# Optimization experiments

Measured on AMD Instinct MI355X. Metric: run time of the kernel, lower is better.

## Reference

```python
import jax, jax.numpy as jnp
import numpy as np

NUM_BINS = 30
MIN_BW = 1e-3
MIN_BH = 1e-3
MIN_D = 1e-3
LO_IN, HI_IN = 0.0, 1.0
LO_OUT, HI_OUT = 0.0, 1.0
DERIV_OUT_LO = (HI_OUT - LO_OUT) / (HI_IN - LO_IN)  # default outside derivatives
DERIV_OUT_HI = DERIV_OUT_LO
EPS = 1e-6
B, V = 65536, 64


def _cumparams(unnorm, lo, hi, min_size):
    # softmax bin sizes with a floor, cumsum into knot positions. [V,K] -> ([V,K+1],[V,K])
    K = unnorm.shape[-1]
    p = jax.nn.softmax(unnorm, axis=-1)
    p = min_size + (1.0 - min_size * K) * p
    cp = jnp.cumsum(p, axis=-1)
    cp = jnp.pad(cp, [(0, 0), (1, 0)])
    cp = (hi - lo) * cp + lo
    cp = cp.at[..., 0].set(lo).at[..., -1].set(hi)
    sizes = cp[..., 1:] - cp[..., :-1]
    return cp, sizes


def setup_inputs() -> dict:
    key = jax.random.key(0)
    k0, k1, k2, k3 = jax.random.split(key, 4)
    return {
        "inputs": jax.random.uniform(k0, (B, V), dtype=jnp.float32),
        "unnormalized_widths": jax.random.uniform(k1, (V, NUM_BINS), dtype=jnp.float32),
        "unnormalized_heights": jax.random.uniform(k2, (V, NUM_BINS), dtype=jnp.float32),
        "unnormalized_derivatives": jax.random.uniform(k3, (V, NUM_BINS - 1), dtype=jnp.float32),
    }


def reference(inputs, unnormalized_widths, unnormalized_heights, unnormalized_derivatives):
    K = NUM_BINS
    nb, nv = inputs.shape

    cumw, widths = _cumparams(unnormalized_widths, LO_IN, HI_IN, MIN_BW)      # [V,K+1],[V,K]
    cumh, heights = _cumparams(unnormalized_heights, LO_OUT, HI_OUT, MIN_BH)  # [V,K+1],[V,K]

    # boundary derivatives pinned so softplus(const)+MIN_D == 1
    const = float(np.log(np.exp(1.0 - MIN_D) - 1.0))
    ud = jnp.pad(unnormalized_derivatives, [(0, 0), (1, 1)], constant_values=const)
    derivs = MIN_D + jax.nn.softplus(ud)  # [V,K+1]
    delta = heights / widths              # [V,K]

    # per-element bin search (forward mode -> search in cumwidths)
    bounds = cumw.at[..., -1].add(EPS)                                   # [V,K+1]
    bin_idx = jnp.sum(inputs[..., None] >= bounds[None], axis=-1) - 1    # [B,V]
    bin_idx = jnp.clip(bin_idx, 0, K - 1)

    vidx = jnp.arange(nv)[None, :]  # broadcast variable index [1,V]
    icw = cumw[vidx, bin_idx]       # input_cumwidths [B,V]
    ibw = widths[vidx, bin_idx]
    ich = cumh[vidx, bin_idx]
    idl = delta[vidx, bin_idx]
    d0 = derivs[vidx, bin_idx]
    d1 = derivs[vidx, bin_idx + 1]
    ih = heights[vidx, bin_idx]

    theta = (inputs - icw) / ibw
    t1mt = theta * (1.0 - theta)
    numerator = ih * (idl * theta * theta + d0 * t1mt)
    denominator = idl + (d0 + d1 - 2.0 * idl) * t1mt
    spline_out = ich + numerator / denominator
    deriv_num = idl * idl * (d1 * theta * theta + 2.0 * idl * t1mt + d0 * (1.0 - theta) ** 2)
    spline_lad = jnp.log(deriv_num) - 2.0 * jnp.log(denominator)

    below = inputs < LO_IN
    above = inputs > HI_IN
    inside = ~(below | above)
    out_lo = LO_OUT + (inputs - LO_IN) * DERIV_OUT_LO
    out_hi = HI_OUT + (inputs - HI_IN) * DERIV_OUT_HI
    outputs = jnp.where(below, out_lo, jnp.where(above, out_hi, spline_out))
    logabsdet = jnp.where(inside, spline_lad, 0.0)
    return outputs, logabsdet
```

## Files before the change

kernel.cpp:

```cpp
#include <hip/hip_runtime.h>
#include <math.h>


#define NB 65536
#define NV 64
#define NKB 30
#define REC_D 124
#define DER_BASE 7936
#define DER_S 33
#define LUT_BASE_B 40192
#define LUT_S 132
#define TOT_D 12160
#define GRID 768
#define BSZ 512

__global__ __launch_bounds__(64) void rqs_params(const float* __restrict__ uw,
                                                 const float* __restrict__ uh,
                                                 const float* __restrict__ ud,
                                                 float* __restrict__ P) {
  const int v = blockIdx.x;
  const int lane = threadIdx.x;
  const float MINB = 1e-3f;
  const float scale = 1.0f - MINB * (float)NKB;

  float cw_e, winv, wnxt;
  {
    float u = (lane < NKB) ? uw[v * NKB + lane] : -1e30f;
    float m = u;
#pragma unroll
    for (int s = 32; s >= 1; s >>= 1) m = fmaxf(m, __shfl_xor(m, s));
    float e = (lane < NKB) ? expf(u - m) : 0.0f;
    float t = e;
#pragma unroll
    for (int s = 32; s >= 1; s >>= 1) t += __shfl_xor(t, s);
    float pk = (lane < NKB) ? (MINB + scale * (e / t)) : 0.0f;
    float ci = pk;
#pragma unroll
    for (int s = 1; s < 64; s <<= 1) {
      float z = __shfl_up(ci, s);
      if (lane >= s) ci += z;
    }
    cw_e = ci - pk;
    wnxt = (lane == NKB - 1) ? 1.0f : ci;
    winv = 1.0f / (wnxt - cw_e);
  }
  float ch_e, hh;
  {
    float u = (lane < NKB) ? uh[v * NKB + lane] : -1e30f;
    float m = u;
#pragma unroll
    for (int s = 32; s >= 1; s >>= 1) m = fmaxf(m, __shfl_xor(m, s));
    float e = (lane < NKB) ? expf(u - m) : 0.0f;
    float t = e;
#pragma unroll
    for (int s = 32; s >= 1; s >>= 1) t += __shfl_xor(t, s);
    float pk = (lane < NKB) ? (MINB + scale * (e / t)) : 0.0f;
    float ci = pk;
#pragma unroll
    for (int s = 1; s < 64; s <<= 1) {
      float z = __shfl_up(ci, s);
      if (lane >= s) ci += z;
    }
    ch_e = ci - pk;
    float hnxt = (lane == NKB - 1) ? 1.0f : ci;
    hh = hnxt - ch_e;
  }
  if (lane < NKB) {
    float4 r = {cw_e, winv, ch_e, hh};
    *(float4*)(P + v * REC_D + 4 * lane) = r;
  }
  if (lane == NKB) {
    float4 r = {1.0f + 1e-6f, 0.0f, 0.0f, 0.0f};
    *(float4*)(P + v * REC_D + 4 * NKB) = r;
  }
  {
    const float CST = (float)log(exp(1.0 - 1e-3) - 1.0);
    if (lane <= NKB) {
      float x = (lane == 0 || lane == NKB) ? CST : ud[v * (NKB - 1) + lane - 1];
      float sp = (x > 0.f) ? (x + log1pf(expf(-x))) : log1pf(expf(x));
      P[DER_BASE + v * DER_S + lane] = 1e-3f + sp;
    }
  }
  {
    float t0 = (float)lane * (1.0f / 128.0f);
    float t1 = (float)(lane + 64) * (1.0f / 128.0f);
    int lo0 = 0, lo1 = 0;
#pragma unroll
    for (int kk = 0; kk < NKB; ++kk) {
      float c = __shfl(wnxt, kk);
      lo0 += (c <= t0) ? 1 : 0;
      lo1 += (c <= t1) ? 1 : 0;
    }
    unsigned char* lb = (unsigned char*)P + LUT_BASE_B + v * LUT_S;
    lb[lane] = (unsigned char)lo0;
    lb[lane + 64] = (unsigned char)lo1;
  }
}

__global__ __launch_bounds__(BSZ, 6) void rqs_main(const float* __restrict__ x,
                                                   const float* __restrict__ P,
                                                   float* __restrict__ out) {
  __shared__ __align__(16) float lds[TOT_D];
  for (int i = threadIdx.x; i < TOT_D / 4; i += BSZ)
    ((float4*)lds)[i] = ((const float4*)P)[i];
  __syncthreads();
  const unsigned char* lutb = (const unsigned char*)lds;

  const int N = NB * NV;
  const int n4 = N / 4;
  for (int gid = blockIdx.x * BSZ + threadIdx.x; gid < n4; gid += GRID * BSZ) {
    float4 xv = ((const float4*)x)[gid];
    const int v0 = (gid & 15) * 4;
    float xs[4] = {xv.x, xv.y, xv.z, xv.w};
    float o[4], l[4];
#pragma unroll
    for (int j = 0; j < 4; ++j) {
      float xx = xs[j];
      const int vj = v0 + j;
      int u = (int)(xx * 128.0f);
      u = u < 0 ? 0 : (u > 127 ? 127 : u);
      int lo = lutb[LUT_BASE_B + vj * LUT_S + u];
      float probe = lds[vj * REC_D + 4 * (lo + 1)];
      int b = lo + ((xx >= probe) ? 1 : 0);
      b = b > 29 ? 29 : b;
      float4 r4 = *(const float4*)&lds[vj * REC_D + 4 * b];
      float d0 = lds[DER_BASE + vj * DER_S + b];
      float d1 = lds[DER_BASE + vj * DER_S + b + 1];
      float icw = r4.x, winv = r4.y, ich = r4.z, ih = r4.w;
      float idl  = ih * winv;
      float th   = (xx - icw) * winv;
      float omt  = 1.0f - th;
      float t1mt = th * omt;
      float th2  = th * th;
      float num  = ih * (idl * th2 + d0 * t1mt);
      float den  = idl + (d0 + d1 - 2.0f * idl) * t1mt;
      float rden = __builtin_amdgcn_rcpf(den);
      float so   = ich + num * rden;
      float dn   = idl * idl * (d1 * th2 + 2.0f * idl * t1mt + d0 * omt * omt);
      float sl   = __logf(dn * rden * rden);
      bool inside = !(xx < 0.0f) && !(xx > 1.0f);
      o[j] = inside ? so : xx;
      l[j] = inside ? sl : 0.0f;
    }
    float4 ov = {o[0], o[1], o[2], o[3]};
    float4 lv = {l[0], l[1], l[2], l[3]};
    ((float4*)out)[gid] = ov;
    ((float4*)(out + N))[gid] = lv;
  }
}

extern "C" void kernel_launch(void* const* d_in, const int* in_sizes, int n_in,
                              void* d_out, int out_size, void* d_ws, size_t ws_size,
                              hipStream_t stream) {
  const float* x  = (const float*)d_in[0];
  const float* uw = (const float*)d_in[1];
  const float* uh = (const float*)d_in[2];
  const float* ud = (const float*)d_in[3];
  float* out = (float*)d_out;
  float* P   = (float*)d_ws;

  rqs_params<<<NV, 64, 0, stream>>>(uw, uh, ud, P);
  rqs_main<<<GRID, BSZ, 0, stream>>>(x, P, out);
}
```

Baseline: 85.40 us.

## Fuse parameter kernel into main kernel and embed knot fraction in LUT

Merges the per-variable parameter kernel into the main kernel, so every block recomputes the softmax, cumsum, softplus and LUT for all 64 variables directly into LDS. This removes a second launch and the global workspace round-trip. Each LUT entry now packs a 16-bit fractional knot position alongside the bin index, so the probe comparison no longer needs a second LDS read. Grid drops to 512 blocks with occupancy hint 4, and per-variable base offsets are hoisted out of the loop. In exchange, each block repeats the parameter work and the LDS footprint grows, and the quantized probe could in rare cases pick a different bin than the exact knot.

```diff
diff --git a/kernel.cpp b/kernel.cpp
--- a/kernel.cpp
+++ b/kernel.cpp
@@ -8,130 +8,146 @@
 #define REC_D 124
 #define DER_BASE 7936
 #define DER_S 33
-#define LUT_BASE_B 40192
-#define LUT_S 132
-#define TOT_D 12160
-#define GRID 768
+#define LUTD_BASE 10048
+#define LUT_S 133
+#define TOT_D 18560
+#define GRID 512
 #define BSZ 512
 
-__global__ __launch_bounds__(64) void rqs_params(const float* __restrict__ uw,
-                                                 const float* __restrict__ uh,
-                                                 const float* __restrict__ ud,
-                                                 float* __restrict__ P) {
-  const int v = blockIdx.x;
-  const int lane = threadIdx.x;
+__global__ __launch_bounds__(BSZ, 4) void rqs_fused(const float* __restrict__ x,
+                                                    const float* __restrict__ uw,
+                                                    const float* __restrict__ uh,
+                                                    const float* __restrict__ ud,
+                                                    float* __restrict__ out) {
+  __shared__ __align__(16) float lds[TOT_D];
+  const int tid = threadIdx.x;
+  const int wave = tid >> 6;
+  const int lane = tid & 63;
+  const int half = lane >> 5;
+  const int hl = lane & 31;
   const float MINB = 1e-3f;
   const float scale = 1.0f - MINB * (float)NKB;
 
-  float cw_e, winv, wnxt;
-  {
-    float u = (lane < NKB) ? uw[v * NKB + lane] : -1e30f;
+  for (int p = 0; p < 4; ++p) {
+    const int v = wave * 8 + p * 2 + half;
+    float u = (hl < NKB) ? uw[v * NKB + hl] : -1e30f;
     float m = u;
 #pragma unroll
-    for (int s = 32; s >= 1; s >>= 1) m = fmaxf(m, __shfl_xor(m, s));
-    float e = (lane < NKB) ? expf(u - m) : 0.0f;
+    for (int s = 16; s >= 1; s >>= 1) m = fmaxf(m, __shfl_xor(m, s));
+    float e = (hl < NKB) ? expf(u - m) : 0.0f;
     float t = e;
 #pragma unroll
-    for (int s = 32; s >= 1; s >>= 1) t += __shfl_xor(t, s);
-    float pk = (lane < NKB) ? (MINB + scale * (e / t)) : 0.0f;
+    for (int s = 16; s >= 1; s >>= 1) t += __shfl_xor(t, s);
+    float pk = (hl < NKB) ? (MINB + scale * (e / t)) : 0.0f;
     float ci = pk;
 #pragma unroll
-    for (int s = 1; s < 64; s <<= 1) {
+    for (int s = 1; s < 32; s <<= 1) {
       float z = __shfl_up(ci, s);
-      if (lane >= s) ci += z;
+      if (hl >= s) ci += z;
     }
-    cw_e = ci - pk;
-    wnxt = (lane == NKB - 1) ? 1.0f : ci;
-    winv = 1.0f / (wnxt - cw_e);
-  }
-  float ch_e, hh;
-  {
-    float u = (lane < NKB) ? uh[v * NKB + lane] : -1e30f;
-    float m = u;
+    float cw_e = ci - pk;
+    float wnxt = (hl == NKB - 1) ? 1.0f : ci;
+    float winv = 1.0f / (wnxt - cw_e);
+    float uhv = (hl < NKB) ? uh[v * NKB + hl] : -1e30f;
+    float mh = uhv;
 #pragma unroll
-    for (int s = 32; s >= 1; s >>= 1) m = fmaxf(m, __shfl_xor(m, s));
-    float e = (lane < NKB) ? expf(u - m) : 0.0f;
-    float t = e;
+    for (int s = 16; s >= 1; s >>= 1) mh = fmaxf(mh, __shfl_xor(mh, s));
+    float eh = (hl < NKB) ? expf(uhv - mh) : 0.0f;
+    float th = eh;
 #pragma unroll
-    for (int s = 32; s >= 1; s >>= 1) t += __shfl_xor(t, s);
-    float pk = (lane < NKB) ? (MINB + scale * (e / t)) : 0.0f;
-    float ci = pk;
+    for (int s = 16; s >= 1; s >>= 1) th += __shfl_xor(th, s);
+    float pkh = (hl < NKB) ? (MINB + scale * (eh / th)) : 0.0f;
+    float cih = pkh;
 #pragma unroll
-    for (int s = 1; s < 64; s <<= 1) {
-      float z = __shfl_up(ci, s);
-      if (lane >= s) ci += z;
+    for (int s = 1; s < 32; s <<= 1) {
+      float z = __shfl_up(cih, s);
+      if (hl >= s) cih += z;
     }
-    ch_e = ci - pk;
-    float hnxt = (lane == NKB - 1) ? 1.0f : ci;
-    hh = hnxt - ch_e;
-  }
-  if (lane < NKB) {
-    float4 r = {cw_e, winv, ch_e, hh};
-    *(float4*)(P + v * REC_D + 4 * lane) = r;
-  }
-  if (lane == NKB) {
-    float4 r = {1.0f + 1e-6f, 0.0f, 0.0f, 0.0f};
-    *(float4*)(P + v * REC_D + 4 * NKB) = r;
-  }
-  {
-    const float CST = (float)log(exp(1.0 - 1e-3) - 1.0);
-    if (lane <= NKB) {
-      float x = (lane == 0 || lane == NKB) ? CST : ud[v * (NKB - 1) + lane - 1];
-      float sp = (x > 0.f) ? (x + log1pf(expf(-x))) : log1pf(expf(x));
-      P[DER_BASE + v * DER_S + lane] = 1e-3f + sp;
+    float ch_e = cih - pkh;
+    float hnxt = (hl == NKB - 1) ? 1.0f : cih;
+    float hh = hnxt - ch_e;
+    if (hl < NKB) {
+      float4 r = {cw_e, winv, ch_e, hh};
+      *(float4*)(lds + v * REC_D + 4 * hl) = r;
+    }
+    {
+      const float CST = (float)log(exp(1.0 - 1e-3) - 1.0);
+      if (hl <= NKB) {
+        float xd = (hl == 0 || hl == NKB) ? CST : ud[v * (NKB - 1) + hl - 1];
+        float sp = (xd > 0.f) ? (xd + log1pf(expf(-xd))) : log1pf(expf(xd));
+        lds[DER_BASE + v * DER_S + hl] = 1e-3f + sp;
+      }
+    }
+    {
+      float tb[4];
+      int lo[4];
+#pragma unroll
+      for (int q = 0; q < 4; ++q) {
+        tb[q] = (float)(hl + 32 * q) * (1.0f / 128.0f);
+        lo[q] = 0;
+      }
+      for (int kk = 0; kk < NKB - 1; ++kk) {
+        float c = __shfl(wnxt, (half << 5) + kk);
+#pragma unroll
+        for (int q = 0; q < 4; ++q) lo[q] += (c <= tb[q]) ? 1 : 0;
+      }
+#pragma unroll
+      for (int q = 0; q < 4; ++q) {
+        int ub = hl + 32 * q;
+        float knot = __shfl(wnxt, (half << 5) + lo[q]);
+        float top = (float)(ub + 1) * (1.0f / 128.0f);
+        int frac;
+        if (knot < top) {
+          frac = (int)((knot * 128.0f - (float)ub) * 65536.0f);
+          frac = frac > 65535 ? 65535 : frac;
+        } else {
+          frac = 65535;
+        }
+        ((unsigned int*)lds)[LUTD_BASE + v * LUT_S + ub] =
+            ((unsigned int)frac << 16) | (unsigned int)lo[q];
+      }
     }
   }
-  {
-    float t0 = (float)lane * (1.0f / 128.0f);
-    float t1 = (float)(lane + 64) * (1.0f / 128.0f);
-    int lo0 = 0, lo1 = 0;
-#pragma unroll
-    for (int kk = 0; kk < NKB; ++kk) {
-      float c = __shfl(wnxt, kk);
-      lo0 += (c <= t0) ? 1 : 0;
-      lo1 += (c <= t1) ? 1 : 0;
-    }
-    unsigned char* lb = (unsigned char*)P + LUT_BASE_B + v * LUT_S;
-    lb[lane] = (unsigned char)lo0;
-    lb[lane + 64] = (unsigned char)lo1;
-  }
-}
-
-__global__ __launch_bounds__(BSZ, 6) void rqs_main(const float* __restrict__ x,
-                                                   const float* __restrict__ P,
-                                                   float* __restrict__ out) {
-  __shared__ __align__(16) float lds[TOT_D];
-  for (int i = threadIdx.x; i < TOT_D / 4; i += BSZ)
-    ((float4*)lds)[i] = ((const float4*)P)[i];
   __syncthreads();
-  const unsigned char* lutb = (const unsigned char*)lds;
 
   const int N = NB * NV;
   const int n4 = N / 4;
-  for (int gid = blockIdx.x * BSZ + threadIdx.x; gid < n4; gid += GRID * BSZ) {
+  const int gid0 = blockIdx.x * BSZ + tid;
+  const int v0 = (gid0 & 15) * 4;
+  int baseR[4], baseD[4], baseL[4];
+#pragma unroll
+  for (int j = 0; j < 4; ++j) {
+    const int vj = v0 + j;
+    baseR[j] = vj * REC_D;
+    baseD[j] = DER_BASE + vj * DER_S;
+    baseL[j] = LUTD_BASE + vj * LUT_S;
+  }
+  const unsigned int* lutu = (const unsigned int*)lds;
+
+  for (int gid = gid0; gid < n4; gid += GRID * BSZ) {
     float4 xv = ((const float4*)x)[gid];
-    const int v0 = (gid & 15) * 4;
     float xs[4] = {xv.x, xv.y, xv.z, xv.w};
     float o[4], l[4];
 #pragma unroll
     for (int j = 0; j < 4; ++j) {
       float xx = xs[j];
-      const int vj = v0 + j;
-      int u = (int)(xx * 128.0f);
-      u = u < 0 ? 0 : (u > 127 ? 127 : u);
-      int lo = lutb[LUT_BASE_B + vj * LUT_S + u];
-      float probe = lds[vj * REC_D + 4 * (lo + 1)];
+      int ui = (int)(xx * 128.0f);
+      ui = ui < 0 ? 0 : (ui > 127 ? 127 : ui);
+      unsigned int en = lutu[baseL[j] + ui];
+      int lo = (int)(en & 0xFFu);
+      float probe = ((float)ui + (float)((en >> 16) + 1u) * (1.0f / 65536.0f)) *
+                    (1.0f / 128.0f);
       int b = lo + ((xx >= probe) ? 1 : 0);
       b = b > 29 ? 29 : b;
-      float4 r4 = *(const float4*)&lds[vj * REC_D + 4 * b];
-      float d0 = lds[DER_BASE + vj * DER_S + b];
-      float d1 = lds[DER_BASE + vj * DER_S + b + 1];
+      float4 r4 = *(const float4*)&lds[baseR[j] + 4 * b];
+      float d0 = lds[baseD[j] + b];
+      float d1 = lds[baseD[j] + b + 1];
       float icw = r4.x, winv = r4.y, ich = r4.z, ih = r4.w;
       float idl  = ih * winv;
-      float th   = (xx - icw) * winv;
-      float omt  = 1.0f - th;
-      float t1mt = th * omt;
-      float th2  = th * th;
+      float thx  = (xx - icw) * winv;
+      float omt  = 1.0f - thx;
+      float t1mt = thx * omt;
+      float th2  = thx * thx;
       float num  = ih * (idl * th2 + d0 * t1mt);
       float den  = idl + (d0 + d1 - 2.0f * idl) * t1mt;
       float rden = __builtin_amdgcn_rcpf(den);
@@ -157,8 +173,7 @@
   const float* uh = (const float*)d_in[2];
   const float* ud = (const float*)d_in[3];
   float* out = (float*)d_out;
-  float* P   = (float*)d_ws;
+  (void)d_ws; (void)ws_size;
 
-  rqs_params<<<NV, 64, 0, stream>>>(uw, uh, ud, P);
-  rqs_main<<<GRID, BSZ, 0, stream>>>(x, P, out);
+  rqs_fused<<<GRID, BSZ, 0, stream>>>(x, uw, uh, ud, out);
 }
```

Result: slower. 96.29 us (+12.8%).
